# Kernel tuning notes

Measured on AMD Instinct MI355X. Metric: run time of the kernel, lower is better.

## Reference

```python
import jax, jax.numpy as jnp
import numpy as np

DIM = 512
WS = 7            # window size
N = WS * WS       # tokens per window
H = 16            # num heads
HD = DIM // H     # head dim
SCALE = HD ** -0.5
B_ = 2048         # batch * num_windows
NW = 64           # windows per image (mask leading dim)


def _relative_position_index():
    coords = np.stack(np.meshgrid(np.arange(WS), np.arange(WS), indexing='ij'))  # [2,WS,WS]
    cf = coords.reshape(2, -1)
    rel = cf[:, :, None] - cf[:, None, :]           # [2,N,N]
    rel = rel.transpose(1, 2, 0)
    rel[:, :, 0] += WS - 1
    rel[:, :, 1] += WS - 1
    rel[:, :, 0] *= 2 * WS - 1
    return rel.sum(-1).astype(np.int32)             # [N,N]

REL_IDX = _relative_position_index()


def setup_inputs() -> dict:
    key = jax.random.key(0)
    ks = jax.random.split(key, 7)
    return {
        'x': jax.random.normal(ks[0], (B_, N, DIM), jnp.float32),
        'mask': jax.random.normal(ks[1], (NW, N, N), jnp.float32),
        'qkv_w': jax.random.normal(ks[2], (DIM, 3 * DIM), jnp.float32) * 0.02,
        'qkv_b': jax.random.normal(ks[3], (3 * DIM,), jnp.float32) * 0.02,
        'proj_w': jax.random.normal(ks[4], (DIM, DIM), jnp.float32) * 0.02,
        'proj_b': jax.random.normal(ks[5], (DIM,), jnp.float32) * 0.02,
        'bias_table': jax.random.normal(ks[6], (169, H), jnp.float32) * 0.02,
    }


def reference(x, mask, qkv_w, qkv_b, proj_w, proj_b, bias_table):
    B, n, c = x.shape
    qkv = x @ qkv_w + qkv_b                              # [B,N,3C]
    qkv = qkv.reshape(B, n, 3, H, HD).transpose(2, 0, 3, 1, 4)  # [3,B,H,N,hd]
    q, k, v = qkv[0], qkv[1], qkv[2]
    attn = jnp.einsum('bhid,bhjd->bhij', q * SCALE, k)   # [B,H,N,N]
    # relative position bias gather: [N*N,H] -> [H,N,N]
    rel_bias = bias_table[REL_IDX.reshape(-1)].reshape(n, n, H).transpose(2, 0, 1)
    attn = attn + rel_bias[None]
    # shifted-window mask add: [B//nW, nW, H, N, N]
    attn = attn.reshape(B // NW, NW, H, n, n) + mask[None, :, None]
    attn = attn.reshape(B, H, n, n)
    attn = jax.nn.softmax(attn, axis=-1)
    out = jnp.einsum('bhij,bhjd->bhid', attn, v)         # [B,H,N,hd]
    out = out.transpose(0, 2, 1, 3).reshape(B, n, c)
    return out @ proj_w + proj_b
```

## Files before the change

### kernel.cpp

```cpp
#include <hip/hip_runtime.h>
#include <cstdint>

#define NTOK  49
#define NHEAD 16
#define HD    32
#define BATCH 2048
#define MTOT  (BATCH*NTOK)
#define SCALE 0.17677669529663687f

typedef float  f32x4  __attribute__((ext_vector_type(4)));
typedef __bf16 bf16x8 __attribute__((ext_vector_type(8)));
typedef __bf16 bf16x4 __attribute__((ext_vector_type(4)));
typedef unsigned int u32;
typedef const u32 __attribute__((address_space(1)))* gas_u32p;
typedef u32 __attribute__((address_space(3)))* las_u32p;

__device__ __forceinline__ void gld16(__bf16* lds, const __bf16* g) {
    __builtin_amdgcn_global_load_lds((gas_u32p)(const void*)g, (las_u32p)(void*)lds, 16, 0, 0);
}


__global__ __launch_bounds__(256) void cvt_x(const float* __restrict__ x,
                                             __bf16* __restrict__ o, long n) {
    long i = ((long)blockIdx.x * 256 + threadIdx.x) * 8;
    if (i >= n) return;
    float4 a = *(const float4*)(x + i);
    float4 b = *(const float4*)(x + i + 4);
    bf16x8 t;
    t[0] = (__bf16)a.x; t[1] = (__bf16)a.y; t[2] = (__bf16)a.z; t[3] = (__bf16)a.w;
    t[4] = (__bf16)b.x; t[5] = (__bf16)b.y; t[6] = (__bf16)b.z; t[7] = (__bf16)b.w;
    *(bf16x8*)(o + i) = t;
}

__global__ __launch_bounds__(256) void prep_w(const float* __restrict__ qkv_w,
                                              const float* __restrict__ proj_w,
                                              const float* __restrict__ qkv_b,
                                              __bf16* __restrict__ wqkv_t,
                                              __bf16* __restrict__ wp_t,
                                              float* __restrict__ qkvb_s) {
    int idx = blockIdx.x * 256 + threadIdx.x;
    if (idx < 1536 * 512) {
        int nn = idx >> 9, kk = idx & 511;
        float v = qkv_w[kk * 1536 + nn];
        if (nn < 512) v *= SCALE;
        wqkv_t[idx] = (__bf16)v;
    } else if (idx < 1536 * 512 + 512 * 512) {
        int j = idx - 1536 * 512;
        int nn = j >> 9, kk = j & 511;
        wp_t[j] = (__bf16)proj_w[kk * 512 + nn];
    } else if (idx < 1536 * 512 + 512 * 512 + 1536) {
        int n = idx - (1536 * 512 + 512 * 512);
        float v = qkv_b[n];
        if (n < 512) v *= SCALE;
        qkvb_s[n] = v;
    }
}

__global__ __launch_bounds__(256) void prep_addm(const float* __restrict__ mask,
                                                 const float* __restrict__ bias_table,
                                                 float* __restrict__ addm) {
    int idx = blockIdx.x * 256 + threadIdx.x;
    int rr   = idx & 3;
    int lane = (idx >> 2) & 63;
    int tile = (idx >> 8) & 15;
    int w    = (idx >> 12) & 63;
    int h    = idx >> 18;
    int mt = tile >> 2, nt = tile & 3;
    int g = lane >> 4, c = lane & 15;
    int i = mt * 16 + g * 4 + rr;
    int j = nt * 16 + c;
    float v;
    if (j >= 49)      v = -1e30f;
    else if (i >= 49) v = 0.f;
    else {
        int ai = (i * 37) >> 8, aj = i - ai * 7;
        int bi = (j * 37) >> 8, bj = j - bi * 7;
        int ridx = (ai - bi + 6) * 13 + (aj - bj + 6);
        v = bias_table[ridx * 16 + h] + mask[(w * 49 + i) * 49 + j];
    }
    addm[idx] = v;
}


template <int MODE>
__global__ __launch_bounds__(256)
void gemm_k512(const __bf16* __restrict__ A, const __bf16* __restrict__ Bt,
               const float* __restrict__ bias, float* __restrict__ outF,
               __bf16* __restrict__ outQK, __bf16* __restrict__ outVT, int N) {
    __shared__ __bf16 a_sh[128 * 32];
    __shared__ __bf16 b_sh[128 * 32];
    const int tid = threadIdx.x;
    const int wid = tid >> 6;
    const int lane = tid & 63;
    const int g = lane >> 4, c = lane & 15;
    const int r = lane >> 2;
    const int c8 = (lane & 3) * 8;
    const long m0 = (long)blockIdx.y * 128;
    const long n0 = (long)blockIdx.x * 128;

    const __bf16* aA = A + (m0 + wid * 32 + r) * 512 + c8;
    const __bf16* aB = Bt + (n0 + wid * 32 + r) * 512 + c8;
    __bf16* lA = a_sh + wid * 32 * 32;
    __bf16* lB = b_sh + wid * 32 * 32;

    f32x4 acc[4][4];
    for (int i = 0; i < 4; ++i)
        for (int j = 0; j < 4; ++j) acc[i][j] = (f32x4){0.f, 0.f, 0.f, 0.f};

    const int wm = (wid >> 1) * 64;
    const int wn = (wid & 1) * 64;

    for (int kt = 0; kt < 16; ++kt) {
        const int ko = kt * 32;
        gld16(lA,           aA + ko);
        gld16(lA + 16 * 32, aA + (long)16 * 512 + ko);
        gld16(lB,           aB + ko);
        gld16(lB + 16 * 32, aB + (long)16 * 512 + ko);
        __syncthreads();
        bf16x8 af[4], bf[4];
        for (int mt = 0; mt < 4; ++mt)
            af[mt] = *(const bf16x8*)(a_sh + (wm + mt * 16 + c) * 32 + g * 8);
        for (int nt = 0; nt < 4; ++nt)
            bf[nt] = *(const bf16x8*)(b_sh + (wn + nt * 16 + c) * 32 + g * 8);
        for (int mt = 0; mt < 4; ++mt)
            for (int nt = 0; nt < 4; ++nt)
                acc[mt][nt] = __builtin_amdgcn_mfma_f32_16x16x32_bf16(af[mt], bf[nt], acc[mt][nt], 0, 0, 0);
        __syncthreads();
    }

    for (int nt = 0; nt < 4; ++nt) {
        const long n = n0 + wn + nt * 16 + c;
        const float bv = bias[n];
        for (int mt = 0; mt < 4; ++mt) {
            const long row0 = m0 + wm + mt * 16 + g * 4;
            if (MODE == 0) {
                for (int rr = 0; rr < 4; ++rr)
                    outF[(row0 + rr) * (long)N + n] = acc[mt][nt][rr] + bv;
            } else if (n0 < 1024) {
                for (int rr = 0; rr < 4; ++rr)
                    outQK[(row0 + rr) * 1024 + n] = (__bf16)(acc[mt][nt][rr] + bv);
            } else {
                const int h = ((int)n - 1024) >> 5;
                const int d = ((int)n - 1024) & 31;
                for (int rr = 0; rr < 4; ++rr) {
                    int row = (int)row0 + rr;
                    int b2 = row / 49;
                    int t2 = row - b2 * 49;
                    outVT[(long)(b2 * 512 + h * 32 + d) * 64 + t2] = (__bf16)(acc[mt][nt][rr] + bv);
                }
            }
        }
    }
}


__global__ __launch_bounds__(256)
void attn_k(const __bf16* __restrict__ qk, const __bf16* __restrict__ vT,
            const float* __restrict__ addm, __bf16* __restrict__ ao) {
    __shared__ __bf16 p_all[4][64 * 72];
    const int tid = threadIdx.x;
    const int wid = tid >> 6;
    const int lane = tid & 63;
    const int g = lane >> 4, c = lane & 15;
    const int wv = blockIdx.x * 4 + wid;
    const int b = wv >> 4, h = wv & 15;
    const int w = b & 63;
    __bf16* psh = p_all[wid];

    const __bf16* base = qk + (long)b * 49 * 1024 + h * 32;

    bf16x8 zero8;
    for (int i = 0; i < 8; ++i) zero8[i] = (__bf16)0.f;

    bf16x8 aq[4], bk[4];
    for (int t4 = 0; t4 < 4; ++t4) {
        int t = t4 * 16 + c;
        const __bf16* p = base + (long)t * 1024 + g * 8;
        bool ok = t < 49;
        aq[t4] = ok ? *(const bf16x8*)p : zero8;
        bk[t4] = ok ? *(const bf16x8*)(p + 512) : zero8;
    }

    const float* am = addm + (long)(h * 64 + w) * 4096;
    f32x4 acc[4][4];
    for (int mt = 0; mt < 4; ++mt)
        for (int nt = 0; nt < 4; ++nt)
            acc[mt][nt] = *(const f32x4*)(am + (mt * 4 + nt) * 256 + lane * 4);

    for (int mt = 0; mt < 4; ++mt)
        for (int nt = 0; nt < 4; ++nt)
            acc[mt][nt] = __builtin_amdgcn_mfma_f32_16x16x32_bf16(aq[mt], bk[nt], acc[mt][nt], 0, 0, 0);

    float linv[4][4];
    for (int mt = 0; mt < 4; ++mt)
        for (int rr = 0; rr < 4; ++rr) {
            float mx = fmaxf(fmaxf(acc[mt][0][rr], acc[mt][1][rr]),
                             fmaxf(acc[mt][2][rr], acc[mt][3][rr]));
            for (int s = 1; s < 16; s <<= 1) mx = fmaxf(mx, __shfl_xor(mx, s));
            float sum = 0.f;
            for (int nt = 0; nt < 4; ++nt) {
                float p = __expf(acc[mt][nt][rr] - mx);
                acc[mt][nt][rr] = p;
                sum += p;
            }
            for (int s = 1; s < 16; s <<= 1) sum += __shfl_xor(sum, s);
            linv[mt][rr] = 1.0f / sum;
        }

    for (int mt = 0; mt < 4; ++mt)
        for (int nt = 0; nt < 4; ++nt)
            for (int rr = 0; rr < 4; ++rr)
                psh[(mt * 16 + g * 4 + rr) * 72 + nt * 16 + c] =
                    (__bf16)(acc[mt][nt][rr] * linv[mt][rr]);

    const __bf16* vb = vT + (long)(b * 16 + h) * 2048;
    bf16x8 av[2][2];
    for (int mt2 = 0; mt2 < 2; ++mt2)
        for (int k2 = 0; k2 < 2; ++k2)
            av[mt2][k2] = *(const bf16x8*)(vb + (mt2 * 16 + c) * 64 + k2 * 32 + g * 8);

    bf16x8 bp[4][2];
    for (int nt2 = 0; nt2 < 4; ++nt2)
        for (int k2 = 0; k2 < 2; ++k2)
            bp[nt2][k2] = *(const bf16x8*)(psh + (nt2 * 16 + c) * 72 + k2 * 32 + g * 8);

    f32x4 oacc[2][4];
    for (int mt2 = 0; mt2 < 2; ++mt2)
        for (int nt2 = 0; nt2 < 4; ++nt2) oacc[mt2][nt2] = (f32x4){0.f, 0.f, 0.f, 0.f};
    for (int mt2 = 0; mt2 < 2; ++mt2)
        for (int nt2 = 0; nt2 < 4; ++nt2)
            for (int k2 = 0; k2 < 2; ++k2)
                oacc[mt2][nt2] = __builtin_amdgcn_mfma_f32_16x16x32_bf16(av[mt2][k2], bp[nt2][k2], oacc[mt2][nt2], 0, 0, 0);

    __bf16* obase = ao + (long)b * 49 * 512 + h * 32;
    for (int nt2 = 0; nt2 < 4; ++nt2) {
        int i = nt2 * 16 + c;
        if (i < 49) {
            for (int mt2 = 0; mt2 < 2; ++mt2) {
                bf16x4 t;
                t[0] = (__bf16)oacc[mt2][nt2][0];
                t[1] = (__bf16)oacc[mt2][nt2][1];
                t[2] = (__bf16)oacc[mt2][nt2][2];
                t[3] = (__bf16)oacc[mt2][nt2][3];
                *(bf16x4*)(obase + (long)i * 512 + mt2 * 16 + g * 4) = t;
            }
        }
    }
}


extern "C" void kernel_launch(void* const* d_in, const int* in_sizes, int n_in,
                              void* d_out, int out_size, void* d_ws, size_t ws_size,
                              hipStream_t stream) {
    const float* x      = (const float*)d_in[0];
    const float* mask   = (const float*)d_in[1];
    const float* qkv_w  = (const float*)d_in[2];
    const float* qkv_b  = (const float*)d_in[3];
    const float* proj_w = (const float*)d_in[4];
    const float* proj_b = (const float*)d_in[5];
    const float* btab   = (const float*)d_in[6];
    float* out = (float*)d_out;

    char* ws = (char*)d_ws;
    __bf16* ws_x   = (__bf16*)ws;
    __bf16* ws_ao  = (__bf16*)ws;
    __bf16* ws_qk  = (__bf16*)(ws + 102760448L);
    __bf16* wqkv_t = (__bf16*)(ws + 308281344L);
    __bf16* wp_t   = (__bf16*)(ws + 309854208L);
    float*  qkvb_s = (float*)(ws + 310378496L);
    float*  addm   = (float*)(ws + 310384640L);
    __bf16* ws_vT  = (__bf16*)(ws + 327161856L);

    const long XN = (long)MTOT * 512;

    cvt_x<<<25088, 256, 0, stream>>>(x, ws_x, XN);
    prep_w<<<4102, 256, 0, stream>>>(qkv_w, proj_w, qkv_b, wqkv_t, wp_t, qkvb_s);
    prep_addm<<<16384, 256, 0, stream>>>(mask, btab, addm);

    gemm_k512<1><<<dim3(12, 784), 256, 0, stream>>>(ws_x, wqkv_t, qkvb_s, nullptr, ws_qk, ws_vT, 1536);
    attn_k<<<8192, 256, 0, stream>>>(ws_qk, ws_vT, addm, ws_ao);
    gemm_k512<0><<<dim3(4, 784), 256, 0, stream>>>(ws_ao, wp_t, proj_b, out, nullptr, nullptr, 512);
}
```

Baseline: 966.7 us.

## Replace GEMM with 256x256 tiled, multi-stage pipelined MFMA kernel

Replaces the 128x128 single-buffered GEMM with a 512-thread 256x256 tile kernel. It prefetches global-to-LDS loads several stages ahead under explicit vmcnt waits and raw barriers, and XOR-swizzles the LDS layout to avoid bank conflicts. It also remaps workgroups for cache locality and raises MFMA priority during compute phases. The aim is to hide memory latency and raise data reuse for both the QKV and projection GEMMs. In exchange it uses more registers and LDS per block, and the hand-written wait counts are fragile to get right.

Result: faster. 905.3 us (-6.4%).

```diff
diff --git a/kernel.cpp b/kernel.cpp
--- a/kernel.cpp
+++ b/kernel.cpp
@@ -82,71 +82,154 @@
 }
 
 
+#define WAIT8 asm volatile("s_waitcnt vmcnt(8)" ::: "memory")
+#define WAIT4 asm volatile("s_waitcnt vmcnt(4)" ::: "memory")
+#define WAIT0 asm volatile("s_waitcnt vmcnt(0)" ::: "memory")
+#define BARR  do { asm volatile("s_barrier" ::: "memory"); \
+                   __builtin_amdgcn_sched_barrier(0); } while (0)
+#define NOOP  do {} while (0)
+
+#define STAGE_A(sdb, skh, kc) do { \
+    gld16(&Asm[sdb][skh][wid * 512],        Ag + (kc)); \
+    gld16(&Asm[sdb][skh][4096 + wid * 512], Ag + 128 * 512 + (kc)); } while (0)
+#define STAGE_B(sdb, skh, kc) do { \
+    gld16(&Bsm[sdb][skh][wid * 512],        Bg + (kc)); \
+    gld16(&Bsm[sdb][skh][4096 + wid * 512], Bg + 128 * 512 + (kc)); } while (0)
+
+#define PHASE(db, kh, mh, STG, WT) do { \
+    const __bf16* ab = &Asm[db][kh][(mh) ? aoff1 : aoff0]; \
+    af[0] = *(const bf16x8*)(ab); \
+    af[1] = *(const bf16x8*)(ab + 512); \
+    af[2] = *(const bf16x8*)(ab + 1024); \
+    af[3] = *(const bf16x8*)(ab + 1536); \
+    if (!(mh)) { \
+        const __bf16* bb = &Bsm[db][kh][boff]; \
+        bfr[0] = *(const bf16x8*)(bb); \
+        bfr[1] = *(const bf16x8*)(bb + 512); \
+        bfr[2] = *(const bf16x8*)(bb + 1024); \
+        bfr[3] = *(const bf16x8*)(bb + 1536); \
+    } \
+    STG; \
+    WT; \
+    BARR; \
+    __builtin_amdgcn_s_setprio(1); \
+    _Pragma("unroll") \
+    for (int mf = 0; mf < 4; ++mf) { \
+        _Pragma("unroll") \
+        for (int nf = 0; nf < 4; ++nf) \
+            acc[(mh) * 4 + mf][nf] = __builtin_amdgcn_mfma_f32_16x16x32_bf16( \
+                af[mf], bfr[nf], acc[(mh) * 4 + mf][nf], 0, 0, 0); \
+    } \
+    __builtin_amdgcn_s_setprio(0); \
+    __builtin_amdgcn_sched_barrier(0); \
+  } while (0)
+
 template <int MODE>
-__global__ __launch_bounds__(256)
-void gemm_k512(const __bf16* __restrict__ A, const __bf16* __restrict__ Bt,
-               const float* __restrict__ bias, float* __restrict__ outF,
-               __bf16* __restrict__ outQK, __bf16* __restrict__ outVT, int N) {
-    __shared__ __bf16 a_sh[128 * 32];
-    __shared__ __bf16 b_sh[128 * 32];
-    const int tid = threadIdx.x;
-    const int wid = tid >> 6;
+__global__ __launch_bounds__(512, 2)
+void gemm256(const __bf16* __restrict__ A, const __bf16* __restrict__ Bt,
+             const float* __restrict__ bias, float* __restrict__ outF,
+             __bf16* __restrict__ outQK, __bf16* __restrict__ outVT, int NBX) {
+    __shared__ __align__(16) __bf16 Asm[2][2][8192];
+    __shared__ __align__(16) __bf16 Bsm[2][2][8192];
+    const int tid  = threadIdx.x;
+    const int wid  = tid >> 6;
     const int lane = tid & 63;
     const int g = lane >> 4, c = lane & 15;
-    const int r = lane >> 2;
-    const int c8 = (lane & 3) * 8;
-    const long m0 = (long)blockIdx.y * 128;
-    const long n0 = (long)blockIdx.x * 128;
-
-    const __bf16* aA = A + (m0 + wid * 32 + r) * 512 + c8;
-    const __bf16* aB = Bt + (n0 + wid * 32 + r) * 512 + c8;
-    __bf16* lA = a_sh + wid * 32 * 32;
-    __bf16* lB = b_sh + wid * 32 * 32;
-
-    f32x4 acc[4][4];
-    for (int i = 0; i < 4; ++i)
+    const int wr = wid >> 2, wc = wid & 3;
+
+    const int nwg = NBX * 392;
+    const int lin = blockIdx.y * NBX + blockIdx.x;
+    const int sw  = (lin & 7) * (nwg >> 3) + (lin >> 3);
+    const int bm  = sw / NBX;
+    const int bn  = sw - bm * NBX;
+    const long m0 = (long)bm * 256;
+    const long n0 = (long)bn * 256;
+
+    const int sr = tid >> 2;
+    const int sl = (tid & 3) ^ ((tid >> 3) & 3);
+    const __bf16* Ag = A  + (m0 + sr) * 512 + sl * 8;
+    const __bf16* Bg = Bt + (n0 + sr) * 512 + sl * 8;
+
+    const int koff  = (g ^ ((c >> 1) & 3)) * 8;
+    const int aoff0 = (wr * 128 + c) * 32 + koff;
+    const int aoff1 = aoff0 + 64 * 32;
+    const int boff  = (wc * 64 + c) * 32 + koff;
+
+    bf16x8 af[4], bfr[4];
+    f32x4 acc[8][4];
+#pragma unroll
+    for (int i = 0; i < 8; ++i)
+#pragma unroll
         for (int j = 0; j < 4; ++j) acc[i][j] = (f32x4){0.f, 0.f, 0.f, 0.f};
 
-    const int wm = (wid >> 1) * 64;
-    const int wn = (wid & 1) * 64;
-
-    for (int kt = 0; kt < 16; ++kt) {
-        const int ko = kt * 32;
-        gld16(lA,           aA + ko);
-        gld16(lA + 16 * 32, aA + (long)16 * 512 + ko);
-        gld16(lB,           aB + ko);
-        gld16(lB + 16 * 32, aB + (long)16 * 512 + ko);
-        __syncthreads();
-        bf16x8 af[4], bf[4];
-        for (int mt = 0; mt < 4; ++mt)
-            af[mt] = *(const bf16x8*)(a_sh + (wm + mt * 16 + c) * 32 + g * 8);
-        for (int nt = 0; nt < 4; ++nt)
-            bf[nt] = *(const bf16x8*)(b_sh + (wn + nt * 16 + c) * 32 + g * 8);
-        for (int mt = 0; mt < 4; ++mt)
-            for (int nt = 0; nt < 4; ++nt)
-                acc[mt][nt] = __builtin_amdgcn_mfma_f32_16x16x32_bf16(af[mt], bf[nt], acc[mt][nt], 0, 0, 0);
-        __syncthreads();
-    }
-
-    for (int nt = 0; nt < 4; ++nt) {
-        const long n = n0 + wn + nt * 16 + c;
-        const float bv = bias[n];
-        for (int mt = 0; mt < 4; ++mt) {
-            const long row0 = m0 + wm + mt * 16 + g * 4;
-            if (MODE == 0) {
+    STAGE_A(0, 0, 0);    STAGE_B(0, 0, 0);
+    STAGE_A(0, 1, 32);   STAGE_B(0, 1, 32);
+    STAGE_A(1, 0, 64);   STAGE_B(1, 0, 64);
+    WAIT8;
+    BARR;
+
+#pragma unroll 1
+    for (int t = 0; t < 6; ++t) {
+        const int db = t & 1, odb = db ^ 1;
+        const int kA = (t + 1) * 64 + 32;
+        const int kB = (t + 2) * 64;
+        PHASE(db, 0, 0, STAGE_A(odb, 1, kA), NOOP);
+        PHASE(db, 0, 1, STAGE_B(odb, 1, kA), WAIT8);
+        PHASE(db, 1, 0, STAGE_A(db, 0, kB),  NOOP);
+        PHASE(db, 1, 1, STAGE_B(db, 0, kB),  WAIT8);
+    }
+    PHASE(0, 0, 0, STAGE_A(1, 1, 480), NOOP);
+    PHASE(0, 0, 1, STAGE_B(1, 1, 480), WAIT8);
+    PHASE(0, 1, 0, NOOP, NOOP);
+    PHASE(0, 1, 1, NOOP, WAIT4);
+    PHASE(1, 0, 0, NOOP, NOOP);
+    PHASE(1, 0, 1, NOOP, WAIT0);
+    PHASE(1, 1, 0, NOOP, NOOP);
+    PHASE(1, 1, 1, NOOP, NOOP);
+
+    if (MODE == 0) {
+#pragma unroll
+        for (int nf = 0; nf < 4; ++nf) {
+            const int n = (int)n0 + wc * 64 + nf * 16 + c;
+            const float bv = bias[n];
+#pragma unroll
+            for (int mi = 0; mi < 8; ++mi) {
+                const long row0 = m0 + wr * 128 + mi * 16 + g * 4;
+#pragma unroll
                 for (int rr = 0; rr < 4; ++rr)
-                    outF[(row0 + rr) * (long)N + n] = acc[mt][nt][rr] + bv;
-            } else if (n0 < 1024) {
+                    outF[(row0 + rr) * 512 + n] = acc[mi][nf][rr] + bv;
+            }
+        }
+    } else if (n0 < 1024) {
+#pragma unroll
+        for (int nf = 0; nf < 4; ++nf) {
+            const int n = (int)n0 + wc * 64 + nf * 16 + c;
+            const float bv = bias[n];
+#pragma unroll
+            for (int mi = 0; mi < 8; ++mi) {
+                const long row0 = m0 + wr * 128 + mi * 16 + g * 4;
+#pragma unroll
                 for (int rr = 0; rr < 4; ++rr)
-                    outQK[(row0 + rr) * 1024 + n] = (__bf16)(acc[mt][nt][rr] + bv);
-            } else {
-                const int h = ((int)n - 1024) >> 5;
-                const int d = ((int)n - 1024) & 31;
+                    outQK[(row0 + rr) * 1024 + n] = (__bf16)(acc[mi][nf][rr] + bv);
+            }
+        }
+    } else {
+#pragma unroll
+        for (int nf = 0; nf < 4; ++nf) {
+            const int n = (int)n0 + wc * 64 + nf * 16 + c;
+            const float bv = bias[n];
+            const int hh = (n - 1024) >> 5;
+            const int dd = (n - 1024) & 31;
+#pragma unroll
+            for (int mi = 0; mi < 8; ++mi) {
+                const int row0 = (int)m0 + wr * 128 + mi * 16 + g * 4;
+#pragma unroll
                 for (int rr = 0; rr < 4; ++rr) {
-                    int row = (int)row0 + rr;
-                    int b2 = row / 49;
-                    int t2 = row - b2 * 49;
-                    outVT[(long)(b2 * 512 + h * 32 + d) * 64 + t2] = (__bf16)(acc[mt][nt][rr] + bv);
+                    const int row = row0 + rr;
+                    const int b2 = row / 49;
+                    const int t2 = row - b2 * 49;
+                    outVT[(long)(b2 * 512 + hh * 32 + dd) * 64 + t2] =
+                        (__bf16)(acc[mi][nf][rr] + bv);
                 }
             }
         }
@@ -277,7 +360,7 @@
     prep_w<<<4102, 256, 0, stream>>>(qkv_w, proj_w, qkv_b, wqkv_t, wp_t, qkvb_s);
     prep_addm<<<16384, 256, 0, stream>>>(mask, btab, addm);
 
-    gemm_k512<1><<<dim3(12, 784), 256, 0, stream>>>(ws_x, wqkv_t, qkvb_s, nullptr, ws_qk, ws_vT, 1536);
+    gemm256<1><<<dim3(6, 392), 512, 0, stream>>>(ws_x, wqkv_t, qkvb_s, nullptr, ws_qk, ws_vT, 6);
     attn_k<<<8192, 256, 0, stream>>>(ws_qk, ws_vT, addm, ws_ao);
-    gemm_k512<0><<<dim3(4, 784), 256, 0, stream>>>(ws_ao, wp_t, proj_b, out, nullptr, nullptr, 512);
-}
+    gemm256<0><<<dim3(2, 392), 512, 0, stream>>>(ws_ao, wp_t, proj_b, out, nullptr, nullptr, 2);
+}
```
